# Performance work log

Measured on AMD Instinct MI355X. Metric: run time of the kernel, lower is better.

Reference implementation:

```python
import jax, jax.numpy as jnp
import numpy as np

N = 10000        # nodes
E = 160000       # edges (avg degree 16)
IN = 8 * 144     # 1152
OUT = 2 * 144    # 288 per ChebConv
KS = [4, 5, 6, 7]


def setup_inputs() -> dict:
    key = jax.random.key(0)
    ks = jax.random.split(key, 10)
    x = jax.random.normal(ks[0], (N, IN), dtype=jnp.float32)
    edge_index = jax.random.randint(ks[1], (2, E), 0, N, dtype=jnp.int32)
    d = {"x": x, "edge_index": edge_index}
    for i, (name, K) in enumerate(zip(["3", "5", "7", "9"], KS)):
        d["W" + name] = jax.random.normal(ks[2 + i], (K, IN, OUT), dtype=jnp.float32) * 0.02
        d["b" + name] = jnp.zeros((OUT,), dtype=jnp.float32)
    return d


def _cheb_basis(x, edge_index, K):
    """Chebyshev basis T_0..T_{K-1} of L_hat = -D^{-1/2} A D^{-1/2} (lambda_max=2,
    as in PyG ChebConv default; self-loop term 2/lambda_max - 1 = 0)."""
    row, col = edge_index[0], edge_index[1]  # source, target
    n = x.shape[0]
    w = jnp.ones(row.shape, x.dtype)
    deg = jax.ops.segment_sum(w, row, num_segments=n)
    dinv = jnp.where(deg > 0, jax.lax.rsqrt(jnp.maximum(deg, 1e-12)), 0.0)
    norm = -(dinv[row] * dinv[col])  # [E]

    def prop(h):  # out[i] = sum_{j->i} norm_e * h[j]
        return jax.ops.segment_sum(h[row] * norm[:, None], col, num_segments=n)

    Tx = [x, prop(x)]
    for _ in range(K - 2):
        Tx.append(2.0 * prop(Tx[-1]) - Tx[-2])
    return jnp.stack(Tx[:K], axis=0)  # [K, N, F]


def reference(x, edge_index, W3, b3, W5, b5, W7, b7, W9, b9):
    T = _cheb_basis(x, edge_index, max(KS))  # shared basis; identical math per conv
    outs = []
    for W, b in ((W3, b3), (W5, b5), (W7, b7), (W9, b9)):
        K = W.shape[0]
        outs.append(jnp.einsum('knf,kfo->no', T[:K], W) + b)
    return jnp.concatenate(outs, axis=1)  # [N, 4*OUT]
```

## Files before the change

### kernel.cpp

```cpp
#include <hip/hip_runtime.h>

#define NN 10000
#define NE 160000
#define FIN 1152
#define FOUT 288
#define FOUT_TOTAL 1152
#define NF (NN * FOUT)
#define WSL (FIN * FOUT)
#define NSLICE 22
#define NMT 79
#define GEMM_BLOCKS 5688

typedef __attribute__((ext_vector_type(8))) short short8;
typedef __attribute__((ext_vector_type(8))) unsigned short ushort8v;
typedef __attribute__((ext_vector_type(4))) float floatx4;

__device__ __forceinline__ unsigned short f2bf(float f) {
  unsigned int u = __float_as_uint(f);
  u += 0x7FFF + ((u >> 16) & 1);
  return (unsigned short)(u >> 16);
}
__device__ __forceinline__ float bf2f(unsigned short u) {
  return __uint_as_float(((unsigned int)u) << 16);
}

__device__ __forceinline__ void async_copy16(void* lds, const void* gmem) {
  __builtin_amdgcn_global_load_lds(
      (const __attribute__((address_space(1))) unsigned int*)gmem,
      (__attribute__((address_space(3))) unsigned int*)lds, 16, 0, 0);
}


__global__ void deg_kernel(const int* __restrict__ ei, int* __restrict__ deg,
                           int* __restrict__ indeg) {
  int e = blockIdx.x * 256 + threadIdx.x;
  if (e < NE) {
    atomicAdd(&deg[ei[e]], 1);
    atomicAdd(&indeg[ei[NE + e]], 1);
  }
}

__global__ void dinv_kernel(const int* __restrict__ deg, float* __restrict__ dinv) {
  int i = blockIdx.x * 256 + threadIdx.x;
  if (i < NN) {
    int d = deg[i];
    dinv[i] = d > 0 ? rsqrtf((float)d) : 0.0f;
  }
}

__global__ __launch_bounds__(256) void scan_kernel(
    const int* __restrict__ indeg, int* __restrict__ rowptr,
    int* __restrict__ cursor) {
  __shared__ int buf[10240];
  __shared__ int sums[256];
  const int t = threadIdx.x;
  for (int i = t; i < 10240; i += 256) buf[i] = (i < NN) ? indeg[i] : 0;
  __syncthreads();
  const int base = t * 40;
  int tot = 0;
#pragma unroll
  for (int j = 0; j < 40; j++) tot += buf[base + j];
  sums[t] = tot;
  __syncthreads();
  for (int off = 1; off < 256; off <<= 1) {
    int v = (t >= off) ? sums[t - off] : 0;
    __syncthreads();
    sums[t] += v;
    __syncthreads();
  }
  int run = sums[t] - tot;
#pragma unroll
  for (int j = 0; j < 40; j++) {
    int v = buf[base + j];
    buf[base + j] = run;
    run += v;
  }
  __syncthreads();
  for (int i = t; i < NN; i += 256) {
    int v = buf[i];
    rowptr[i] = v;
    cursor[i] = v;
  }
  if (t == 255) rowptr[NN] = sums[255];
}

__global__ void scatter_kernel(const int* __restrict__ ei, const float* __restrict__ dinv,
                               int* __restrict__ cursor, int* __restrict__ srcarr,
                               float* __restrict__ wn) {
  int e = blockIdx.x * 256 + threadIdx.x;
  if (e < NE) {
    int r = ei[e], c = ei[NE + e];
    int pos = atomicAdd(&cursor[c], 1);
    srcarr[pos] = r;
    wn[pos] = -(dinv[r] * dinv[c]);
  }
}

__global__ __launch_bounds__(256) void wtrans_kernel(
    const float* __restrict__ W0, const float* __restrict__ W1,
    const float* __restrict__ W2, const float* __restrict__ W3,
    unsigned short* __restrict__ Wt) {
  __shared__ float tile[32][33];
  const int s = blockIdx.y;
  int c, k;
  if (s < 4)       { c = 0; k = s; }
  else if (s < 9)  { c = 1; k = s - 4; }
  else if (s < 15) { c = 2; k = s - 9; }
  else             { c = 3; k = s - 15; }
  const float* W = ((c == 0) ? W0 : (c == 1) ? W1 : (c == 2) ? W2 : W3) +
                   (size_t)k * WSL;
  const int bx = blockIdx.x;
  const int f0 = (bx % 36) * 32;
  const int o0 = (bx / 36) * 32;
  const int tx = threadIdx.x & 31;
  const int ty = threadIdx.x >> 5;
#pragma unroll
  for (int jj = 0; jj < 4; jj++)
    tile[ty + 8 * jj][tx] = W[(size_t)(f0 + ty + 8 * jj) * FOUT + (o0 + tx)];
  __syncthreads();
  unsigned short* dst = Wt + (size_t)s * WSL;
#pragma unroll
  for (int jj = 0; jj < 4; jj++)
    dst[(size_t)(o0 + ty + 8 * jj) * FIN + (f0 + tx)] = f2bf(tile[tx][ty + 8 * jj]);
}

__global__ void xcast_kernel(const float* __restrict__ x, unsigned short* __restrict__ xb) {
  int i = blockIdx.x * 256 + threadIdx.x;
  if (i < NN * FIN / 4) {
    float4 v = *(const float4*)(x + (size_t)i * 4);
    ushort4 r;
    r.x = f2bf(v.x); r.y = f2bf(v.y); r.z = f2bf(v.z); r.w = f2bf(v.w);
    *(ushort4*)(xb + (size_t)i * 4) = r;
  }
}

__global__ __launch_bounds__(256) void gemm_mfma_kernel(
    const unsigned short* __restrict__ Xb, const unsigned short* __restrict__ Wt,
    unsigned short* __restrict__ Yall, int Lofs) {
  const int L = Lofs + blockIdx.x;
  const int j = L & 7;
  const int m = L >> 3;
  const int nsl = (j < 6) ? 3 : 2;
  const int work = nsl * 3 * NMT;
  if (m >= work) return;
  const int mtile = m / (nsl * 3);
  const int rem = m - mtile * (nsl * 3);
  const int slice = j + 8 * (rem / 3);
  const int n0 = (rem % 3) * 96;
  const int m0 = mtile * 128;

  __shared__ unsigned short As[128][64];
  __shared__ unsigned short Bs[96][64];

  const int tid = threadIdx.x;
  const int lane = tid & 63;
  const int wave = tid >> 6;
  const int wx = wave & 1;
  const int wy = wave >> 1;
  const int lm = lane & 15;
  const int hi = lane >> 4;

  floatx4 acc[4][3];
#pragma unroll
  for (int i = 0; i < 4; i++)
#pragma unroll
    for (int jj = 0; jj < 3; jj++) acc[i][jj] = (floatx4){0.f, 0.f, 0.f, 0.f};

  const unsigned short* Wbase = Wt + (size_t)slice * WSL;

  for (int f0 = 0; f0 < FIN; f0 += 64) {
    __syncthreads();
#pragma unroll
    for (int i = 0; i < 4; i++) {
      int idx = i * 256 + tid;
      int row = idx >> 3;
      int ck = idx & 7;
      int gr = m0 + row;
      gr = gr < NN ? gr : NN - 1;
      async_copy16((char*)&As[0][0] + idx * 16,
                   (const char*)Xb + ((size_t)gr * FIN + f0) * 2 + ((ck ^ (row & 7)) << 4));
    }
#pragma unroll
    for (int i = 0; i < 3; i++) {
      int idx = i * 256 + tid;
      int row = idx >> 3;
      int ck = idx & 7;
      async_copy16((char*)&Bs[0][0] + idx * 16,
                   (const char*)Wbase + ((size_t)(n0 + row) * FIN + f0) * 2 + ((ck ^ (row & 7)) << 4));
    }
    __syncthreads();
#pragma unroll
    for (int s = 0; s < 2; s++) {
      short8 a[4], b[3];
#pragma unroll
      for (int i = 0; i < 4; i++) {
        int ar = wy * 64 + i * 16 + lm;
        a[i] = *(const short8*)((const char*)&As[ar][0] + (((s * 4 + hi) ^ (ar & 7)) << 4));
      }
#pragma unroll
      for (int jj = 0; jj < 3; jj++) {
        int br = wx * 48 + jj * 16 + lm;
        b[jj] = *(const short8*)((const char*)&Bs[br][0] + (((s * 4 + hi) ^ (br & 7)) << 4));
      }
#pragma unroll
      for (int i = 0; i < 4; i++)
#pragma unroll
        for (int jj = 0; jj < 3; jj++)
          acc[i][jj] = __builtin_amdgcn_mfma_f32_16x16x32_bf16(a[i], b[jj], acc[i][jj], 0, 0, 0);
    }
  }
  unsigned short* Yb = Yall + (size_t)slice * NF;
  const int cbase = n0 + wx * 48 + lm;
  const int rbase = (lane >> 4) * 4;
#pragma unroll
  for (int i = 0; i < 4; i++) {
#pragma unroll
    for (int r = 0; r < 4; r++) {
      int grow = m0 + wy * 64 + i * 16 + rbase + r;
      if (grow < NN) {
        unsigned short* op = Yb + (size_t)grow * FOUT + cbase;
#pragma unroll
        for (int jj = 0; jj < 3; jj++) op[jj * 16] = f2bf(acc[i][jj][r]);
      }
    }
  }
}


struct StepA {
  const unsigned short* H[4];
  const unsigned short* Y[4];
  const unsigned short* P[4];
  unsigned short* D[4];
};

template <int NACT>
__global__ __launch_bounds__(576) void cl_step_fused(
    StepA a, const int* __restrict__ rowptr, const int* __restrict__ srcarr,
    const float* __restrict__ wn) {
  const int t = threadIdx.x;
  const int ln = t % 36;
  const int node = blockIdx.x * 16 + t / 36;
  if (node >= NN) return;
  const int off = ln * 8;
  const int rs = rowptr[node];
  const int re = rowptr[node + 1];
  float acc[NACT][8];
#pragma unroll
  for (int s = 0; s < NACT; s++)
#pragma unroll
    for (int q = 0; q < 8; q++) acc[s][q] = 0.f;

  constexpr int U = (NACT <= 2) ? 4 : 2;
  int p = rs;
  for (; p + U <= re; p += U) {
    int r[U];
    float w[U];
#pragma unroll
    for (int u = 0; u < U; u++) { r[u] = srcarr[p + u]; w[u] = wn[p + u]; }
    ushort8v h[U][NACT];
#pragma unroll
    for (int u = 0; u < U; u++)
#pragma unroll
      for (int s = 0; s < NACT; s++)
        h[u][s] = *(const ushort8v*)(a.H[s] + (size_t)r[u] * FOUT + off);
#pragma unroll
    for (int u = 0; u < U; u++)
#pragma unroll
      for (int s = 0; s < NACT; s++)
#pragma unroll
        for (int q = 0; q < 8; q++) acc[s][q] += w[u] * bf2f(h[u][s][q]);
  }
  for (; p < re; ++p) {
    int r = srcarr[p];
    float w = wn[p];
#pragma unroll
    for (int s = 0; s < NACT; s++) {
      ushort8v hh = *(const ushort8v*)(a.H[s] + (size_t)r * FOUT + off);
#pragma unroll
      for (int q = 0; q < 8; q++) acc[s][q] += w * bf2f(hh[q]);
    }
  }

  size_t o = (size_t)node * FOUT + off;
#pragma unroll
  for (int s = 0; s < NACT; s++) {
    ushort8v y = *(const ushort8v*)(a.Y[s] + o);
    ushort8v d;
    if (a.P[s]) {
      ushort8v pp = *(const ushort8v*)(a.P[s] + o);
#pragma unroll
      for (int q = 0; q < 8; q++) d[q] = f2bf(bf2f(y[q]) + 2.f * acc[s][q] - bf2f(pp[q]));
    } else {
#pragma unroll
      for (int q = 0; q < 8; q++) d[q] = f2bf(bf2f(y[q]) + 2.f * acc[s][q]);
    }
    *(ushort8v*)(a.D[s] + o) = d;
  }
}

struct FinalA {
  const unsigned short* H[4];
  const unsigned short* Y[4];
  const unsigned short* P[4];
  const float* B[4];
  int conv[4];
};

__global__ __launch_bounds__(576) void cl_final_fused(
    FinalA a, const int* __restrict__ rowptr, const int* __restrict__ srcarr,
    const float* __restrict__ wn, float* __restrict__ out) {
  const int t = threadIdx.x;
  const int ln = t % 36;
  const int node = blockIdx.x * 16 + t / 36;
  if (node >= NN) return;
  const int off = ln * 8;
  const int rs = rowptr[node];
  const int re = rowptr[node + 1];
  float acc[4][8];
#pragma unroll
  for (int s = 0; s < 4; s++)
#pragma unroll
    for (int q = 0; q < 8; q++) acc[s][q] = 0.f;

  constexpr int U = 2;
  int p = rs;
  for (; p + U <= re; p += U) {
    int r[U];
    float w[U];
#pragma unroll
    for (int u = 0; u < U; u++) { r[u] = srcarr[p + u]; w[u] = wn[p + u]; }
    ushort8v h[U][4];
#pragma unroll
    for (int u = 0; u < U; u++)
#pragma unroll
      for (int s = 0; s < 4; s++)
        h[u][s] = *(const ushort8v*)(a.H[s] + (size_t)r[u] * FOUT + off);
#pragma unroll
    for (int u = 0; u < U; u++)
#pragma unroll
      for (int s = 0; s < 4; s++)
#pragma unroll
        for (int q = 0; q < 8; q++) acc[s][q] += w[u] * bf2f(h[u][s][q]);
  }
  for (; p < re; ++p) {
    int r = srcarr[p];
    float w = wn[p];
#pragma unroll
    for (int s = 0; s < 4; s++) {
      ushort8v hh = *(const ushort8v*)(a.H[s] + (size_t)r * FOUT + off);
#pragma unroll
      for (int q = 0; q < 8; q++) acc[s][q] += w * bf2f(hh[q]);
    }
  }

  size_t o = (size_t)node * FOUT + off;
#pragma unroll
  for (int s = 0; s < 4; s++) {
    ushort8v y = *(const ushort8v*)(a.Y[s] + o);
    ushort8v pp = *(const ushort8v*)(a.P[s] + o);
    const float* bias = a.B[s] + off;
    float r8[8];
#pragma unroll
    for (int q = 0; q < 8; q++)
      r8[q] = bias[q] + bf2f(y[q]) + acc[s][q] - bf2f(pp[q]);
    float* op = out + (size_t)node * FOUT_TOTAL + a.conv[s] * FOUT + off;
    *(float4*)(op + 0) = make_float4(r8[0], r8[1], r8[2], r8[3]);
    *(float4*)(op + 4) = make_float4(r8[4], r8[5], r8[6], r8[7]);
  }
}


extern "C" void kernel_launch(void* const* d_in, const int* in_sizes, int n_in,
                              void* d_out, int out_size, void* d_ws, size_t ws_size,
                              hipStream_t stream) {
  const float* x = (const float*)d_in[0];
  const int* ei = (const int*)d_in[1];
  const float* W[4] = {(const float*)d_in[2], (const float*)d_in[4],
                       (const float*)d_in[6], (const float*)d_in[8]};
  const float* b[4] = {(const float*)d_in[3], (const float*)d_in[5],
                       (const float*)d_in[7], (const float*)d_in[9]};
  float* out = (float*)d_out;

  char* ws = (char*)d_ws;
  size_t off = 0;
  auto alloc = [&](size_t bytes) -> char* {
    char* p = ws + off;
    off += (bytes + 255) & ~(size_t)255;
    return p;
  };
  int* deg = (int*)alloc(NN * 4);
  int* indeg = (int*)alloc(NN * 4);
  int* rowptr = (int*)alloc((NN + 1) * 4);
  int* cursor = (int*)alloc(NN * 4);
  int* srcarr = (int*)alloc(NE * 4);
  float* wn = (float*)alloc(NE * 4);
  float* dinv = (float*)alloc(NN * 4);
  unsigned short* xb = (unsigned short*)alloc((size_t)NN * FIN * 2);
  unsigned short* Wt = (unsigned short*)alloc((size_t)NSLICE * WSL * 2);
  unsigned short* Yall = (unsigned short*)alloc((size_t)NSLICE * NF * 2);

  hipMemsetAsync(deg, 0, NN * 4, stream);
  hipMemsetAsync(indeg, 0, NN * 4, stream);

  deg_kernel<<<(NE + 255) / 256, 256, 0, stream>>>(ei, deg, indeg);
  dinv_kernel<<<(NN + 255) / 256, 256, 0, stream>>>(deg, dinv);
  scan_kernel<<<1, 256, 0, stream>>>(indeg, rowptr, cursor);
  scatter_kernel<<<(NE + 255) / 256, 256, 0, stream>>>(ei, dinv, cursor, srcarr, wn);
  wtrans_kernel<<<dim3(324, NSLICE), 256, 0, stream>>>(W[0], W[1], W[2], W[3], Wt);
  xcast_kernel<<<(NN * FIN / 4 + 255) / 256, 256, 0, stream>>>(x, xb);

  {
    const int chunk = GEMM_BLOCKS / 3;
    gemm_mfma_kernel<<<chunk, 256, 0, stream>>>(xb, Wt, Yall, 0);
    gemm_mfma_kernel<<<chunk, 256, 0, stream>>>(xb, Wt, Yall, chunk);
    gemm_mfma_kernel<<<chunk, 256, 0, stream>>>(xb, Wt, Yall, 2 * chunk);
  }

  const int nK[4] = {4, 5, 6, 7};
  const int st[4] = {0, 4, 9, 15};
  unsigned short* S[4];
  for (int c = 0; c < 4; c++) S[c] = xb + (size_t)c * NF;

  StepA sched[5];
  int nact[5] = {0, 0, 0, 0, 0};
  FinalA fa;

  for (int c = 3; c >= 0; c--) {
    int n = nK[c] - 1;
    int s0 = 6 - n;
    unsigned short* Yn = Yall + (size_t)(st[c] + n) * NF;
    unsigned short* A = S[c];
    for (int p = 1; p <= n; p++) {
      int s = s0 + p - 1;
      if (p < n) {
        unsigned short* H = (p & 1) ? Yn : A;
        unsigned short* D = (p & 1) ? A : Yn;
        int j = nact[s]++;
        sched[s].H[j] = H;
        sched[s].Y[j] = Yall + (size_t)(st[c] + n - p) * NF;
        sched[s].P[j] = (p == 1) ? nullptr : D;
        sched[s].D[j] = D;
      } else {
        int j = 3 - c;
        fa.H[j] = ((n - 1) & 1) ? A : Yn;
        fa.P[j] = ((n - 2) & 1) ? A : Yn;
        fa.Y[j] = Yall + (size_t)st[c] * NF;
        fa.B[j] = b[c];
        fa.conv[j] = c;
      }
    }
  }

  for (int s = 0; s < 5; s++)
    for (int j = nact[s]; j < 4; j++) {
      sched[s].H[j] = sched[s].H[0];
      sched[s].Y[j] = sched[s].Y[0];
      sched[s].P[j] = sched[s].P[0];
      sched[s].D[j] = sched[s].D[0];
    }

  const int grid_cl = NN / 16;
  for (int s = 0; s < 5; s++) {
    switch (nact[s]) {
      case 1: cl_step_fused<1><<<grid_cl, 576, 0, stream>>>(sched[s], rowptr, srcarr, wn); break;
      case 2: cl_step_fused<2><<<grid_cl, 576, 0, stream>>>(sched[s], rowptr, srcarr, wn); break;
      case 3: cl_step_fused<3><<<grid_cl, 576, 0, stream>>>(sched[s], rowptr, srcarr, wn); break;
      default: cl_step_fused<4><<<grid_cl, 576, 0, stream>>>(sched[s], rowptr, srcarr, wn); break;
    }
  }
  cl_final_fused<<<grid_cl, 576, 0, stream>>>(fa, rowptr, srcarr, wn, out);
}
```

Baseline: 680.2 us.

## Split each node's edge list across two lanes and merge GEMM launches

The Chebyshev propagation kernels now give each node 72 threads instead of 36. The two lanes that share a feature chunk each sum half of the node's edge list, and the halves are combined with a lane shuffle before one lane writes the result. This doubles the grid and the gather parallelism per node, which aims to expose more memory-level parallelism and shorten per-thread dependency chains, at the cost of extra shuffles and idle lanes in the epilogue. The three chunked GEMM launches are also folded into a single launch to save launch overhead.

```diff
diff --git a/kernel.cpp b/kernel.cpp
--- a/kernel.cpp
+++ b/kernel.cpp
@@ -136,8 +136,8 @@
 
 __global__ __launch_bounds__(256) void gemm_mfma_kernel(
     const unsigned short* __restrict__ Xb, const unsigned short* __restrict__ Wt,
-    unsigned short* __restrict__ Yall, int Lofs) {
-  const int L = Lofs + blockIdx.x;
+    unsigned short* __restrict__ Yall) {
+  const int L = blockIdx.x;
   const int j = L & 7;
   const int m = L >> 3;
   const int nsl = (j < 6) ? 3 : 2;
@@ -239,12 +239,17 @@
     StepA a, const int* __restrict__ rowptr, const int* __restrict__ srcarr,
     const float* __restrict__ wn) {
   const int t = threadIdx.x;
-  const int ln = t % 36;
-  const int node = blockIdx.x * 16 + t / 36;
-  if (node >= NN) return;
+  const int nodesub = t / 72;
+  const int rem = t - nodesub * 72;
+  const int ln = rem >> 1;
+  const int half = rem & 1;
+  const int node = blockIdx.x * 8 + nodesub;
   const int off = ln * 8;
-  const int rs = rowptr[node];
-  const int re = rowptr[node + 1];
+  const int rs0 = rowptr[node];
+  const int re0 = rowptr[node + 1];
+  const int mid = rs0 + ((re0 - rs0 + 1) >> 1);
+  const int rs = half ? mid : rs0;
+  const int re = half ? re0 : mid;
   float acc[NACT][8];
 #pragma unroll
   for (int s = 0; s < NACT; s++)
@@ -282,20 +287,28 @@
     }
   }
 
-  size_t o = (size_t)node * FOUT + off;
-#pragma unroll
-  for (int s = 0; s < NACT; s++) {
-    ushort8v y = *(const ushort8v*)(a.Y[s] + o);
-    ushort8v d;
-    if (a.P[s]) {
-      ushort8v pp = *(const ushort8v*)(a.P[s] + o);
-#pragma unroll
-      for (int q = 0; q < 8; q++) d[q] = f2bf(bf2f(y[q]) + 2.f * acc[s][q] - bf2f(pp[q]));
-    } else {
-#pragma unroll
-      for (int q = 0; q < 8; q++) d[q] = f2bf(bf2f(y[q]) + 2.f * acc[s][q]);
-    }
-    *(ushort8v*)(a.D[s] + o) = d;
+#pragma unroll
+  for (int s = 0; s < NACT; s++)
+#pragma unroll
+    for (int q = 0; q < 8; q++) acc[s][q] += __shfl_xor(acc[s][q], 1, 64);
+
+  if (half == 0) {
+    size_t o = (size_t)node * FOUT + off;
+#pragma unroll
+    for (int s = 0; s < NACT; s++) {
+      ushort8v y = *(const ushort8v*)(a.Y[s] + o);
+      ushort8v d;
+      if (a.P[s]) {
+        ushort8v pp = *(const ushort8v*)(a.P[s] + o);
+#pragma unroll
+        for (int q = 0; q < 8; q++)
+          d[q] = f2bf(bf2f(y[q]) + 2.f * acc[s][q] - bf2f(pp[q]));
+      } else {
+#pragma unroll
+        for (int q = 0; q < 8; q++) d[q] = f2bf(bf2f(y[q]) + 2.f * acc[s][q]);
+      }
+      *(ushort8v*)(a.D[s] + o) = d;
+    }
   }
 }
 
@@ -311,12 +324,17 @@
     FinalA a, const int* __restrict__ rowptr, const int* __restrict__ srcarr,
     const float* __restrict__ wn, float* __restrict__ out) {
   const int t = threadIdx.x;
-  const int ln = t % 36;
-  const int node = blockIdx.x * 16 + t / 36;
-  if (node >= NN) return;
+  const int nodesub = t / 72;
+  const int rem = t - nodesub * 72;
+  const int ln = rem >> 1;
+  const int half = rem & 1;
+  const int node = blockIdx.x * 8 + nodesub;
   const int off = ln * 8;
-  const int rs = rowptr[node];
-  const int re = rowptr[node + 1];
+  const int rs0 = rowptr[node];
+  const int re0 = rowptr[node + 1];
+  const int mid = rs0 + ((re0 - rs0 + 1) >> 1);
+  const int rs = half ? mid : rs0;
+  const int re = half ? re0 : mid;
   float acc[4][8];
 #pragma unroll
   for (int s = 0; s < 4; s++)
@@ -354,19 +372,26 @@
     }
   }
 
-  size_t o = (size_t)node * FOUT + off;
-#pragma unroll
-  for (int s = 0; s < 4; s++) {
-    ushort8v y = *(const ushort8v*)(a.Y[s] + o);
-    ushort8v pp = *(const ushort8v*)(a.P[s] + o);
-    const float* bias = a.B[s] + off;
-    float r8[8];
-#pragma unroll
-    for (int q = 0; q < 8; q++)
-      r8[q] = bias[q] + bf2f(y[q]) + acc[s][q] - bf2f(pp[q]);
-    float* op = out + (size_t)node * FOUT_TOTAL + a.conv[s] * FOUT + off;
-    *(float4*)(op + 0) = make_float4(r8[0], r8[1], r8[2], r8[3]);
-    *(float4*)(op + 4) = make_float4(r8[4], r8[5], r8[6], r8[7]);
+#pragma unroll
+  for (int s = 0; s < 4; s++)
+#pragma unroll
+    for (int q = 0; q < 8; q++) acc[s][q] += __shfl_xor(acc[s][q], 1, 64);
+
+  if (half == 0) {
+    size_t o = (size_t)node * FOUT + off;
+#pragma unroll
+    for (int s = 0; s < 4; s++) {
+      ushort8v y = *(const ushort8v*)(a.Y[s] + o);
+      ushort8v pp = *(const ushort8v*)(a.P[s] + o);
+      const float* bias = a.B[s] + off;
+      float r8[8];
+#pragma unroll
+      for (int q = 0; q < 8; q++)
+        r8[q] = bias[q] + bf2f(y[q]) + acc[s][q] - bf2f(pp[q]);
+      float* op = out + (size_t)node * FOUT_TOTAL + a.conv[s] * FOUT + off;
+      *(float4*)(op + 0) = make_float4(r8[0], r8[1], r8[2], r8[3]);
+      *(float4*)(op + 4) = make_float4(r8[4], r8[5], r8[6], r8[7]);
+    }
   }
 }
 
@@ -410,12 +435,7 @@
   wtrans_kernel<<<dim3(324, NSLICE), 256, 0, stream>>>(W[0], W[1], W[2], W[3], Wt);
   xcast_kernel<<<(NN * FIN / 4 + 255) / 256, 256, 0, stream>>>(x, xb);
 
-  {
-    const int chunk = GEMM_BLOCKS / 3;
-    gemm_mfma_kernel<<<chunk, 256, 0, stream>>>(xb, Wt, Yall, 0);
-    gemm_mfma_kernel<<<chunk, 256, 0, stream>>>(xb, Wt, Yall, chunk);
-    gemm_mfma_kernel<<<chunk, 256, 0, stream>>>(xb, Wt, Yall, 2 * chunk);
-  }
+  gemm_mfma_kernel<<<GEMM_BLOCKS, 256, 0, stream>>>(xb, Wt, Yall);
 
   const int nK[4] = {4, 5, 6, 7};
   const int st[4] = {0, 4, 9, 15};
@@ -460,7 +480,7 @@
       sched[s].D[j] = sched[s].D[0];
     }
 
-  const int grid_cl = NN / 16;
+  const int grid_cl = NN / 8;
   for (int s = 0; s < 5; s++) {
     switch (nact[s]) {
       case 1: cl_step_fused<1><<<grid_cl, 576, 0, stream>>>(sched[s], rowptr, srcarr, wn); break;
```

After: 657.1 us. 1.04x faster.
